# Performance work log

Measured on AMD Instinct MI355X. Metric: run time of the kernel, lower is better.

The kernel has to match this reference:

```python
import jax, jax.numpy as jnp
import numpy as np

DIM = 256
N_CHANNELS = 8
NEIGHBORS = 16


def setup_inputs() -> dict:
    key = jax.random.key(0)
    kx, kw = jax.random.split(key)
    B, N, D = 4, 1024, DIM
    x = jax.random.normal(kx, (B, N, D), dtype=jnp.float32)
    # nn.Linear(dim, dim*2*n_channels, bias=False); store as [in, out] so y = x @ W
    W_qk = jax.random.normal(kw, (D, 2 * N_CHANNELS * D), dtype=jnp.float32) * (D ** -0.5)
    return {"x": x, "W_qk": W_qk}


def _norm_edge(edge):
    # edge: [B, C, N, N]
    norm_row = edge / (edge.sum(axis=-1, keepdims=True) + 1e-6)
    norm_col = norm_row / (norm_row.sum(axis=-2, keepdims=True) + 1e-6)
    # norm_row @ norm_col^T
    return jnp.einsum('bcnk,bcmk->bcnm', norm_row, norm_col)


def reference(x, W_qk):
    B, N, D = x.shape
    C = N_CHANNELS
    scale = D ** -0.5
    qk = (x @ W_qk).reshape(B, N, 2, C, D)
    q = jnp.transpose(qk[:, :, 0], (0, 2, 1, 3))  # [B, C, N, D]
    k = jnp.transpose(qk[:, :, 1], (0, 2, 1, 3))  # [B, C, N, D]
    attn = jax.nn.softmax(jnp.einsum('bcnd,bcmd->bcnm', q, k) * scale, axis=-1)

    # clip(): top-k neighbor mask from channel-summed (detached) attention
    sum_edge = jax.lax.stop_gradient(attn).sum(axis=1)  # [B, N, N]
    kk = min(NEIGHBORS, N)
    _, top_idx = jax.lax.top_k(sum_edge, kk)  # [B, N, kk]
    b_idx = jnp.arange(B)[:, None, None]
    r_idx = jnp.arange(N)[None, :, None]
    mask = jnp.zeros((B, N, N), dtype=attn.dtype).at[b_idx, r_idx, top_idx].set(1.0)
    mask = jnp.maximum(mask, jnp.eye(N, dtype=attn.dtype))  # identity diag
    edge = mask[:, None] * attn  # [B, C, N, N]
    return _norm_edge(edge)
```

## Files before the change

### kernel.cpp

```cpp
#include <hip/hip_runtime.h>
#include <hip/hip_bf16.h>
#include <math.h>

#define BB 4
#define NN 1024
#define DD 256
#define CC 8
#define KNBR 16
#define MAXSEL 17
#define ZCAP (NN * MAXSEL)

typedef _Float16 f16x8_t __attribute__((ext_vector_type(8)));
typedef _Float16 f16x4_t __attribute__((ext_vector_type(4)));
typedef _Float16 f16x2_t __attribute__((ext_vector_type(2)));
typedef float    f32x4_t __attribute__((ext_vector_type(4)));

__device__ __forceinline__ void gl2lds16(const _Float16* g, _Float16* ldsbase) {
    __builtin_amdgcn_global_load_lds(
        (const __attribute__((address_space(1))) unsigned int*)g,
        (__attribute__((address_space(3))) unsigned int*)ldsbase, 16, 0, 0);
}

__device__ __forceinline__ void split2(float v, _Float16& h, _Float16& l) {
    h = (_Float16)v;
    l = (_Float16)(v - (float)h);
}

__global__ __launch_bounds__(256) void split_all(const float* __restrict__ x,
                                                 const float* __restrict__ W,
                                                 _Float16* __restrict__ xh,
                                                 _Float16* __restrict__ xl,
                                                 _Float16* __restrict__ Wth,
                                                 _Float16* __restrict__ Wtl,
                                                 int* __restrict__ countb) {
    const int tid = threadIdx.x;
    if (blockIdx.x < 1024) {
        int i = (blockIdx.x * 256 + tid) * 4;
        float4 v = *(const float4*)(x + i);
        f16x4_t hv, lv;
        _Float16 h, l;
        split2(v.x, h, l); hv[0] = h; lv[0] = l;
        split2(v.y, h, l); hv[1] = h; lv[1] = l;
        split2(v.z, h, l); hv[2] = h; lv[2] = l;
        split2(v.w, h, l); hv[3] = h; lv[3] = l;
        *(f16x4_t*)(xh + i) = hv;
        *(f16x4_t*)(xl + i) = lv;
    } else {
        const int b2 = blockIdx.x - 1024;
        if (b2 == 0) {
            int4 zz = make_int4(0, 0, 0, 0);
#pragma unroll
            for (int g = 0; g < 4; g++) ((int4*)countb)[tid + 256 * g] = zz;
        }
        __shared__ float t[64][65];
        const int n0 = (b2 & 63) * 64;
        const int k0 = (b2 >> 6) * 64;
#pragma unroll
        for (int i = 0; i < 16; i++) {
            int k = i * 4 + (tid >> 6);
            int n = tid & 63;
            t[k][n] = W[(size_t)(k0 + k) * 4096 + n0 + n];
        }
        __syncthreads();
#pragma unroll
        for (int i = 0; i < 16; i++) {
            int n = i * 4 + (tid >> 6);
            int k = tid & 63;
            _Float16 h, l;
            split2(t[k][n] * 16.f, h, l);
            size_t o = (size_t)(n0 + n) * 256 + k0 + k;
            Wth[o] = h; Wtl[o] = l;
        }
    }
}

#define STG(dst, src, rowbase, kk)                                             \
    do {                                                                       \
        gl2lds16((src) + (size_t)((rowbase) + r_st) * 256 + (kk) + c8,         \
                 &(dst)[(w * 64) * 8]);                                        \
        gl2lds16((src) + (size_t)((rowbase) + 64 + r_st) * 256 + (kk) + c8,    \
                 &(dst)[(256 + w * 64) * 8]);                                  \
    } while (0)

#define MFMA3(accv, AH, AL, BH, BL)                                            \
    do {                                                                       \
        accv = __builtin_amdgcn_mfma_f32_16x16x32_f16(AL, BH, accv, 0, 0, 0);  \
        accv = __builtin_amdgcn_mfma_f32_16x16x32_f16(AH, BL, accv, 0, 0, 0);  \
        accv = __builtin_amdgcn_mfma_f32_16x16x32_f16(AH, BH, accv, 0, 0, 0);  \
    } while (0)

#define COMPUTE(AH, AL, BH, BL)                                                \
    do {                                                                       \
        f16x8_t ah[4], al[4];                                                  \
        _Pragma("unroll")                                                      \
        for (int mi = 0; mi < 4; mi++) {                                       \
            int r = (wr * 64 + mi * 16 + lm) * 32 + qx8;                       \
            ah[mi] = *(const f16x8_t*)&(AH)[r];                                \
            al[mi] = *(const f16x8_t*)&(AL)[r];                                \
        }                                                                      \
        _Pragma("unroll")                                                      \
        for (int ni = 0; ni < 4; ni++) {                                       \
            int rb = (wc * 64 + ni * 16 + lm) * 32 + qx8;                      \
            f16x8_t bh = *(const f16x8_t*)&(BH)[rb];                           \
            f16x8_t bl = *(const f16x8_t*)&(BL)[rb];                           \
            _Pragma("unroll")                                                  \
            for (int mi = 0; mi < 4; mi++)                                     \
                MFMA3(acc[mi][ni], ah[mi], al[mi], bh, bl);                    \
        }                                                                      \
    } while (0)

__global__ __launch_bounds__(256) void gemm_xw_mfma(
        const _Float16* __restrict__ xh, const _Float16* __restrict__ xl,
        const _Float16* __restrict__ wth, const _Float16* __restrict__ wtl,
        _Float16* __restrict__ qh, _Float16* __restrict__ ql,
        _Float16* __restrict__ kh, _Float16* __restrict__ kl) {
    __shared__ __align__(16) char smem[65536];
    _Float16* Ah0 = (_Float16*)smem;
    _Float16* Al0 = (_Float16*)(smem + 8192);
    _Float16* Bh0 = (_Float16*)(smem + 16384);
    _Float16* Bl0 = (_Float16*)(smem + 24576);
    _Float16* Ah1 = (_Float16*)(smem + 32768);
    _Float16* Al1 = (_Float16*)(smem + 40960);
    _Float16* Bh1 = (_Float16*)(smem + 49152);
    _Float16* Bl1 = (_Float16*)(smem + 57344);
    const int tid = threadIdx.x, lane = tid & 63, w = tid >> 6;
    const int wr = w >> 1, wc = w & 1;
    const int lm = lane & 15, quad = lane >> 4;
    const int row0 = blockIdx.y * 128, col0 = blockIdx.x * 128;
    const int r_st = tid >> 2;
    const int c8 = (((tid & 3) ^ ((tid >> 3) & 3)) * 8);
    const int qx8 = ((quad ^ ((lm >> 1) & 3)) * 8);

    f32x4_t acc[4][4];
#pragma unroll
    for (int i = 0; i < 4; i++)
#pragma unroll
        for (int j = 0; j < 4; j++) acc[i][j] = (f32x4_t)(0.f);

    STG(Ah0, xh, row0, 0); STG(Al0, xl, row0, 0);
    STG(Bh0, wth, col0, 0); STG(Bl0, wtl, col0, 0);
    __syncthreads();
#pragma unroll
    for (int t = 0; t < 8; t += 2) {
        {
            int kn = (t + 1) * 32;
            if (t + 1 < 8) {
                STG(Ah1, xh, row0, kn); STG(Al1, xl, row0, kn);
                STG(Bh1, wth, col0, kn); STG(Bl1, wtl, col0, kn);
            }
            COMPUTE(Ah0, Al0, Bh0, Bl0);
            __syncthreads();
        }
        {
            int kn = (t + 2) * 32;
            if (t + 2 < 8) {
                STG(Ah0, xh, row0, kn); STG(Al0, xl, row0, kn);
                STG(Bh0, wth, col0, kn); STG(Bl0, wtl, col0, kn);
            }
            COMPUTE(Ah1, Al1, Bh1, Bl1);
            __syncthreads();
        }
    }

    float* tr = (float*)smem;
    const int s = col0 >> 11, c = (col0 >> 8) & 7, dbase = col0 & 255;
    _Float16* dh = s ? kh : qh;
    _Float16* dl = s ? kl : ql;
    const int rl = tid >> 2;
    const int cb = (tid & 3) * 8;
#pragma unroll
    for (int p = 0; p < 2; p++) {
        if (p) __syncthreads();
        if (wr == p) {
#pragma unroll
            for (int mi = 0; mi < 4; mi++) {
                int rloc = mi * 16 + quad * 4;
#pragma unroll
                for (int ni = 0; ni < 4; ni++) {
                    int cl = wc * 64 + ni * 16 + lm;
#pragma unroll
                    for (int r = 0; r < 4; r++)
                        tr[(rloc + r) * 132 + cl] = acc[mi][ni][r];
                }
            }
        }
        __syncthreads();
        int rr = row0 + p * 64 + rl;
        int bb = rr >> 10, n = rr & 1023;
        size_t base = (((size_t)(bb * CC + c)) * NN + n) * DD + dbase;
#pragma unroll
        for (int g = 0; g < 4; g++) {
            int ccol = g * 32 + cb;
            f16x8_t hv, lv;
#pragma unroll
            for (int e = 0; e < 8; e++) {
                float vv = tr[rl * 132 + ccol + e];
                _Float16 h, l;
                split2(vv, h, l);
                hv[e] = h; lv[e] = l;
            }
            *(f16x8_t*)(dh + base + ccol) = hv;
            *(f16x8_t*)(dl + base + ccol) = lv;
        }
    }
}

__global__ __launch_bounds__(256) void gemm_qkt_mfma(
        const _Float16* __restrict__ qh, const _Float16* __restrict__ ql,
        const _Float16* __restrict__ kh, const _Float16* __restrict__ kl,
        float* __restrict__ attn) {
    __shared__ __align__(16) char smem[65536];
    _Float16* Ah0 = (_Float16*)smem;
    _Float16* Al0 = (_Float16*)(smem + 8192);
    _Float16* Bh0 = (_Float16*)(smem + 16384);
    _Float16* Bl0 = (_Float16*)(smem + 24576);
    _Float16* Ah1 = (_Float16*)(smem + 32768);
    _Float16* Al1 = (_Float16*)(smem + 40960);
    _Float16* Bh1 = (_Float16*)(smem + 49152);
    _Float16* Bl1 = (_Float16*)(smem + 57344);
    const int tid = threadIdx.x, lane = tid & 63, w = tid >> 6;
    const int wr = w >> 1, wc = w & 1;
    const int lm = lane & 15, quad = lane >> 4;
    const int id = blockIdx.x;
    const int rb8 = id & 7, qq = id >> 3;
    const int j = qq & 63, zhi = qq >> 6;
    const int z = zhi * 8 + rb8;
    const int row0 = (j >> 3) * 128, col0 = (j & 7) * 128;
    const size_t zo = (size_t)z * NN * DD;
    float* Cm = attn + (size_t)z * NN * NN;
    const int r_st = tid >> 2;
    const int c8 = (((tid & 3) ^ ((tid >> 3) & 3)) * 8);
    const int qx8 = ((quad ^ ((lm >> 1) & 3)) * 8);
    const float scale = 0.0625f / 256.0f;

    f32x4_t acc[4][4];
#pragma unroll
    for (int i = 0; i < 4; i++)
#pragma unroll
        for (int j2 = 0; j2 < 4; j2++) acc[i][j2] = (f32x4_t)(0.f);

    const _Float16* qhz = qh + zo;
    const _Float16* qlz = ql + zo;
    const _Float16* khz = kh + zo;
    const _Float16* klz = kl + zo;

    STG(Ah0, qhz, row0, 0); STG(Al0, qlz, row0, 0);
    STG(Bh0, khz, col0, 0); STG(Bl0, klz, col0, 0);
    __syncthreads();
#pragma unroll
    for (int t = 0; t < 8; t += 2) {
        {
            int kn = (t + 1) * 32;
            if (t + 1 < 8) {
                STG(Ah1, qhz, row0, kn); STG(Al1, qlz, row0, kn);
                STG(Bh1, khz, col0, kn); STG(Bl1, klz, col0, kn);
            }
            COMPUTE(Ah0, Al0, Bh0, Bl0);
            __syncthreads();
        }
        {
            int kn = (t + 2) * 32;
            if (t + 2 < 8) {
                STG(Ah0, qhz, row0, kn); STG(Al0, qlz, row0, kn);
                STG(Bh0, khz, col0, kn); STG(Bl0, klz, col0, kn);
            }
            COMPUTE(Ah1, Al1, Bh1, Bl1);
            __syncthreads();
        }
    }

#pragma unroll
    for (int mi = 0; mi < 4; mi++)
#pragma unroll
        for (int ni = 0; ni < 4; ni++) {
            int row = row0 + wr * 64 + mi * 16 + quad * 4;
            int col = col0 + wc * 64 + ni * 16 + lm;
#pragma unroll
            for (int r = 0; r < 4; r++)
                Cm[(size_t)(row + r) * NN + col] = acc[mi][ni][r] * scale;
        }
}

__global__ __launch_bounds__(256) void softmax_topk(const float* __restrict__ attn,
                                                    float2* __restrict__ ml,
                                                    int* __restrict__ idx,
                                                    int* __restrict__ cnt,
                                                    int* __restrict__ countb,
                                                    float* __restrict__ colsum) {
    __shared__ float psum[4][1280];
    __shared__ int fsel[MAXSEL];
    __shared__ int fcnt;
    const int bn = blockIdx.x, b = bn >> 10, n = bn & 1023;
    const int tid = threadIdx.x, lane = tid & 63, w = tid >> 6;

    if (tid < CC) colsum[(size_t)(b * CC + tid) * NN + n] = 0.f;

    const int colb = lane * 16;
    const int pb   = lane * 20;
    float4 u[2][4];
#pragma unroll
    for (int p = 0; p < 2; p++) {
        const int c = w * 2 + p;
        const float* rowp = attn + (((size_t)(b * CC + c) * NN + n) * NN) + colb;
#pragma unroll
        for (int g = 0; g < 4; g++) u[p][g] = *(const float4*)(rowp + g * 4);
    }

    float acc[16];
#pragma unroll
    for (int e = 0; e < 16; e++) acc[e] = 0.f;

#pragma unroll
    for (int p = 0; p < 2; p++) {
        const int c = w * 2 + p;
        const float* f = (const float*)&u[p][0];
        float mx = f[0];
#pragma unroll
        for (int e = 1; e < 16; e++) mx = fmaxf(mx, f[e]);
#pragma unroll
        for (int off = 1; off < 64; off <<= 1) mx = fmaxf(mx, __shfl_xor(mx, off));
        float sm = 0.f;
        float pe[16];
#pragma unroll
        for (int e = 0; e < 16; e++) { pe[e] = expf(f[e] - mx); sm += pe[e]; }
#pragma unroll
        for (int off = 1; off < 64; off <<= 1) sm += __shfl_xor(sm, off);
        if (lane == 0) ml[(size_t)(b * CC + c) * NN + n] = make_float2(mx, sm);
        float inv = 1.0f / sm;
#pragma unroll
        for (int e = 0; e < 16; e++) acc[e] += pe[e] * inv;
    }
#pragma unroll
    for (int g = 0; g < 4; g++)
        *(float4*)&psum[w][pb + g * 4] =
            make_float4(acc[g * 4], acc[g * 4 + 1], acc[g * 4 + 2], acc[g * 4 + 3]);
    __syncthreads();

    const int p4 = tid * 4 + (tid >> 2) * 4;
    float4 a0 = *(const float4*)&psum[0][p4];
    float4 a1 = *(const float4*)&psum[1][p4];
    float4 a2 = *(const float4*)&psum[2][p4];
    float4 a3 = *(const float4*)&psum[3][p4];
    float4 vs;
    vs.x = a0.x + a1.x + a2.x + a3.x;
    vs.y = a0.y + a1.y + a2.y + a3.y;
    vs.z = a0.z + a1.z + a2.z + a3.z;
    vs.w = a0.w + a1.w + a2.w + a3.w;
    *(float4*)&psum[0][p4] = vs;
    __syncthreads();

    if (w == 0) {
        unsigned vb[16];
#pragma unroll
        for (int g = 0; g < 4; g++) {
            float4 t4 = *(const float4*)&psum[0][pb + g * 4];
            vb[g * 4 + 0] = __float_as_uint(t4.x);
            vb[g * 4 + 1] = __float_as_uint(t4.y);
            vb[g * 4 + 2] = __float_as_uint(t4.z);
            vb[g * 4 + 3] = __float_as_uint(t4.w);
        }
        unsigned lo = 0u, hi = 0x7F800000u;
        while (lo < hi) {
            unsigned mid = lo + ((hi - lo) >> 1);
            int c = 0;
#pragma unroll
            for (int e = 0; e < 16; e++)
                c += (int)__popcll(__ballot(vb[e] > mid));
            if (c <= 15) hi = mid; else lo = mid + 1;
        }
        const unsigned V = hi;
        int cgt = 0, ceq = 0;
#pragma unroll
        for (int e = 0; e < 16; e++) {
            cgt += (vb[e] > V) ? 1 : 0;
            ceq += (vb[e] == V) ? 1 : 0;
        }
        int pk = cgt | (ceq << 16);
        int incl = pk;
#pragma unroll
        for (int o = 1; o < 64; o <<= 1) {
            int v2 = __shfl_up(incl, o);
            if (lane >= o) incl += v2;
        }
        int tot = __shfl(incl, 63);
        int c1 = tot & 0xffff;
        int need = KNBR - c1;
        int excl = incl - pk;
        int pg = excl & 0xffff;
        int pe2 = excl >> 16;
        int lg = 0, le = 0;
#pragma unroll
        for (int e = 0; e < 16; e++) {
            if (vb[e] > V) {
                fsel[pg + lg] = colb + e; lg++;
            } else if (vb[e] == V) {
                if (pe2 + le < need) fsel[c1 + pe2 + le] = colb + e;
                le++;
            }
        }
        if (lane == 0) {
            bool has = false;
#pragma unroll
            for (int t2 = 0; t2 < KNBR; t2++)
                if (fsel[t2] == n) has = true;
            int c = KNBR;
            if (!has) { fsel[KNBR] = n; c = KNBR + 1; }
            fcnt = c;
            cnt[bn] = c;
        }
    }
    __syncthreads();
    if (tid < fcnt) {
        idx[bn * MAXSEL + tid] = fsel[tid];
        atomicAdd(&countb[b * NN + fsel[tid]], 1);
    }
}

__global__ __launch_bounds__(256) void scan_offb(const int* __restrict__ countb,
                                                 int* __restrict__ offb,
                                                 int* __restrict__ curs) {
    __shared__ int wtot[4];
    const int b = blockIdx.x, tid = threadIdx.x, lane = tid & 63, w = tid >> 6;
    int c0 = countb[b * NN + tid * 4 + 0];
    int c1 = countb[b * NN + tid * 4 + 1];
    int c2 = countb[b * NN + tid * 4 + 2];
    int c3 = countb[b * NN + tid * 4 + 3];
    int tsum = c0 + c1 + c2 + c3;
    int incl = tsum;
#pragma unroll
    for (int off = 1; off < 64; off <<= 1) {
        int v = __shfl_up(incl, off);
        if (lane >= off) incl += v;
    }
    if (lane == 63) wtot[w] = incl;
    __syncthreads();
    int woff = 0;
    for (int i = 0; i < w; i++) woff += wtot[i];
    int base = woff + incl - tsum;
    int o0 = base, o1 = base + c0, o2 = base + c0 + c1, o3 = base + c0 + c1 + c2;
    offb[b * NN + tid * 4 + 0] = o0;
    offb[b * NN + tid * 4 + 1] = o1;
    offb[b * NN + tid * 4 + 2] = o2;
    offb[b * NN + tid * 4 + 3] = o3;
    curs[b * NN + tid * 4 + 0] = o0;
    curs[b * NN + tid * 4 + 1] = o1;
    curs[b * NN + tid * 4 + 2] = o2;
    curs[b * NN + tid * 4 + 3] = o3;
}

__global__ __launch_bounds__(64) void fill_struct(const int* __restrict__ cnt,
                                                  const int* __restrict__ idx,
                                                  int* __restrict__ curs,
                                                  unsigned short* __restrict__ eidx16,
                                                  int* __restrict__ pmap) {
    const int b = blockIdx.x >> 4;
    const int n = ((blockIdx.x & 15) << 6) + threadIdx.x;
    const int bn = b * NN + n;
    const int c_ = cnt[bn];
    const int start = n & 15;
    for (int jj = 0; jj < MAXSEL; jj++) {
        if (jj < c_) {
            int j = jj + start;
            if (j >= c_) j -= c_;
            int k = idx[bn * MAXSEL + j];
            int p = atomicAdd(&curs[b * NN + k], 1);
            eidx16[b * ZCAP + p] = (unsigned short)n;
            pmap[bn * MAXSEL + j] = p;
        }
    }
}

__global__ __launch_bounds__(256) void rownorm_fill(const float* __restrict__ attn,
                                                    const float2* __restrict__ ml,
                                                    const int* __restrict__ idx,
                                                    const int* __restrict__ cnt,
                                                    const int* __restrict__ pmap,
                                                    float* __restrict__ nr,
                                                    float* __restrict__ colsum,
                                                    _Float16* __restrict__ eval8h) {
    const int t = blockIdx.x * 256 + threadIdx.x;
    const int z = t >> 10, n = t & 1023;
    const int b = z >> 3, c = z & 7;
    const int bn = b * NN + n;
    const int c_ = cnt[bn];
    const float* arow = attn + (size_t)t * NN;
    const float2 MM = ml[t];
    const float invl = 1.0f / MM.y;
    float a[MAXSEL];
    int kk[MAXSEL];
    float s = 0.f;
#pragma unroll
    for (int j = 0; j < MAXSEL; j++) {
        if (j < c_) {
            kk[j] = idx[bn * MAXSEL + j];
            float p = expf(arow[kk[j]] - MM.x) * invl;
            a[j] = p; s += p;
        }
    }
    const float inv = 1.f / (s + 1e-6f);
#pragma unroll
    for (int j = 0; j < MAXSEL; j++) {
        if (j < c_) {
            float v = a[j] * inv;
            nr[(size_t)t * MAXSEL + j] = v;
            atomicAdd(&colsum[(size_t)z * NN + kk[j]], v);
            int p = pmap[bn * MAXSEL + j];
            eval8h[((size_t)b * ZCAP + p) * 8 + c] = (_Float16)v;
        }
    }
}

__global__ __launch_bounds__(512) void out_sparse(const float* __restrict__ nr,
                                                  const int* __restrict__ idx,
                                                  const int* __restrict__ cnt,
                                                  const int* __restrict__ offb,
                                                  const int* __restrict__ countb,
                                                  const float* __restrict__ colsum,
                                                  const unsigned short* __restrict__ eidx16,
                                                  const _Float16* __restrict__ eval8h,
                                                  float* __restrict__ out) {
    __shared__ unsigned accP[NN * 5];
    __shared__ float scm[CC][MAXSEL];
    __shared__ int goffs[MAXSEL];
    __shared__ int glens[MAXSEL];
    const int bn = blockIdx.x;
    const int b = bn >> 10, n = bn & 1023;
    const int tid = threadIdx.x, lane = tid & 63, w = tid >> 6;
    const int c_ = cnt[bn];

#pragma unroll
    for (int q = 0; q < 10; q++) accP[tid + q * 512] = 0u;

    if (tid < 256) {
        int c = tid >> 5, j = tid & 31;
        if (j < MAXSEL) {
            float sc = 0.f;
            if (j < c_) {
                int z = b * CC + c;
                int k = idx[bn * MAXSEL + j];
                float wgt = nr[((size_t)z * NN + n) * MAXSEL + j];
                sc = wgt / (colsum[(size_t)z * NN + k] + 1e-6f);
            }
            scm[c][j] = sc;
        }
    } else if (tid < 256 + MAXSEL) {
        int j = tid - 256;
        int off = 0, len = 0;
        if (j < c_) {
            int k = idx[bn * MAXSEL + j];
            off = offb[b * NN + k];
            len = countb[b * NN + k];
        }
        goffs[j] = off; glens[j] = len;
    }
    __syncthreads();

    for (int j = w; j < c_; j += 8) {
        const int off = goffs[j], len = glens[j];
        f16x8_t scv;
#pragma unroll
        for (int c = 0; c < 8; c++) scv[c] = (_Float16)scm[c][j];
        for (int l = lane; l < len; l += 64) {
            int m = eidx16[b * ZCAP + off + l];
            f16x8_t vh = *(const f16x8_t*)(eval8h + ((size_t)b * ZCAP + off + l) * 8);
            f16x8_t pr = vh * scv;
            const unsigned* pw = (const unsigned*)&pr;
            unsigned base = (unsigned)(uintptr_t)&accP[m * 5];
            asm volatile("ds_pk_add_f16 %0, %1"           :: "v"(base), "v"(pw[0]) : "memory");
            asm volatile("ds_pk_add_f16 %0, %1 offset:4"  :: "v"(base), "v"(pw[1]) : "memory");
            asm volatile("ds_pk_add_f16 %0, %1 offset:8"  :: "v"(base), "v"(pw[2]) : "memory");
            asm volatile("ds_pk_add_f16 %0, %1 offset:12" :: "v"(base), "v"(pw[3]) : "memory");
        }
    }
    __syncthreads();

#pragma unroll
    for (int q = 0; q < 4; q++) {
        int i4 = tid + q * 512;
        int c = i4 >> 8, m0 = (i4 & 255) * 4;
        int p = c >> 1, hi = c & 1;
        float4 vo;
        float* vp = (float*)&vo;
#pragma unroll
        for (int e = 0; e < 4; e++) {
            unsigned wrd = accP[(m0 + e) * 5 + p];
            f16x2_t h2 = *(const f16x2_t*)&wrd;
            vp[e] = (float)h2[hi];
        }
        *(float4*)(out + ((size_t)(b * CC + c) * NN + n) * NN + m0) = vo;
    }
}

extern "C" void kernel_launch(void* const* d_in, const int* in_sizes, int n_in,
                              void* d_out, int out_size, void* d_ws, size_t ws_size,
                              hipStream_t stream) {
    const float* x = (const float*)d_in[0];
    const float* W = (const float*)d_in[1];
    float* out = (float*)d_out;
    char* ws = (char*)d_ws;

    float* attn = (float*)d_out;

    _Float16* qh  = (_Float16*)(ws);
    _Float16* ql  = (_Float16*)(ws + 16777216ull);
    _Float16* kh  = (_Float16*)(ws + 33554432ull);
    _Float16* kl  = (_Float16*)(ws + 50331648ull);
    _Float16* xh  = (_Float16*)(ws + 67108864ull);
    _Float16* xl  = (_Float16*)(ws + 69206016ull);
    _Float16* wth = (_Float16*)(ws + 71303168ull);
    _Float16* wtl = (_Float16*)(ws + 73400320ull);
    int*    idx  = (int*)   (ws + 75497472ull);
    int*    cnt  = (int*)   (ws + 75776000ull);
    float*  nr   = (float*) (ws + 75792384ull);
    float*  colsum = (float*)(ws + 78020608ull);
    float2* ml   = (float2*)(ws + 78151680ull);
    int*    countb = (int*) (ws + 78413824ull);
    int*    offb = (int*)   (ws + 78430208ull);
    int*    curs = (int*)   (ws + 78446592ull);
    unsigned short* eidx16 = (unsigned short*)(ws + 78462976ull);
    _Float16* eval8h = (_Float16*)(ws + 78602240ull);
    int*    pmap = (int*)   (ws + 79716352ull);

    split_all<<<1280, 256, 0, stream>>>(x, W, xh, xl, wth, wtl, countb);
    gemm_xw_mfma<<<dim3(32, 32), 256, 0, stream>>>(xh, xl, wth, wtl,
                                                   qh, ql, kh, kl);
    gemm_qkt_mfma<<<2048, 256, 0, stream>>>(qh, ql, kh, kl, attn);
    softmax_topk<<<4096, 256, 0, stream>>>(attn, ml, idx, cnt, countb, colsum);
    scan_offb<<<4, 256, 0, stream>>>(countb, offb, curs);
    fill_struct<<<64, 64, 0, stream>>>(cnt, idx, curs, eidx16, pmap);
    rownorm_fill<<<128, 256, 0, stream>>>(attn, ml, idx, cnt, pmap, nr, colsum,
                                          eval8h);
    out_sparse<<<4096, 512, 0, stream>>>(nr, idx, cnt, offb, countb, colsum,
                                         eidx16, eval8h, out);
}
```

Before: 360.4 us.

## Process one attention row per wavefront in softmax_topk, dropping LDS reduction

```diff
diff --git a/kernel.cpp b/kernel.cpp
--- a/kernel.cpp
+++ b/kernel.cpp
@@ -287,23 +287,20 @@
                                                     int* __restrict__ cnt,
                                                     int* __restrict__ countb,
                                                     float* __restrict__ colsum) {
-    __shared__ float psum[4][1280];
-    __shared__ int fsel[MAXSEL];
-    __shared__ int fcnt;
-    const int bn = blockIdx.x, b = bn >> 10, n = bn & 1023;
+    __shared__ int fsel[4][MAXSEL];
     const int tid = threadIdx.x, lane = tid & 63, w = tid >> 6;
-
-    if (tid < CC) colsum[(size_t)(b * CC + tid) * NN + n] = 0.f;
+    const int bn = blockIdx.x * 4 + w;
+    const int b = bn >> 10, n = bn & 1023;
+
+    if (lane < CC) colsum[(size_t)(b * CC + lane) * NN + n] = 0.f;
 
     const int colb = lane * 16;
-    const int pb   = lane * 20;
-    float4 u[2][4];
-#pragma unroll
-    for (int p = 0; p < 2; p++) {
-        const int c = w * 2 + p;
+    float4 u[CC][4];
+#pragma unroll
+    for (int c = 0; c < CC; c++) {
         const float* rowp = attn + (((size_t)(b * CC + c) * NN + n) * NN) + colb;
 #pragma unroll
-        for (int g = 0; g < 4; g++) u[p][g] = *(const float4*)(rowp + g * 4);
+        for (int g = 0; g < 4; g++) u[c][g] = *(const float4*)(rowp + g * 4);
     }
 
     float acc[16];
@@ -311,9 +308,8 @@
     for (int e = 0; e < 16; e++) acc[e] = 0.f;
 
 #pragma unroll
-    for (int p = 0; p < 2; p++) {
-        const int c = w * 2 + p;
-        const float* f = (const float*)&u[p][0];
+    for (int c = 0; c < CC; c++) {
+        const float* f = (const float*)&u[c][0];
         float mx = f[0];
 #pragma unroll
         for (int e = 1; e < 16; e++) mx = fmaxf(mx, f[e]);
@@ -330,89 +326,64 @@
 #pragma unroll
         for (int e = 0; e < 16; e++) acc[e] += pe[e] * inv;
     }
-#pragma unroll
-    for (int g = 0; g < 4; g++)
-        *(float4*)&psum[w][pb + g * 4] =
-            make_float4(acc[g * 4], acc[g * 4 + 1], acc[g * 4 + 2], acc[g * 4 + 3]);
-    __syncthreads();
-
-    const int p4 = tid * 4 + (tid >> 2) * 4;
-    float4 a0 = *(const float4*)&psum[0][p4];
-    float4 a1 = *(const float4*)&psum[1][p4];
-    float4 a2 = *(const float4*)&psum[2][p4];
-    float4 a3 = *(const float4*)&psum[3][p4];
-    float4 vs;
-    vs.x = a0.x + a1.x + a2.x + a3.x;
-    vs.y = a0.y + a1.y + a2.y + a3.y;
-    vs.z = a0.z + a1.z + a2.z + a3.z;
-    vs.w = a0.w + a1.w + a2.w + a3.w;
-    *(float4*)&psum[0][p4] = vs;
-    __syncthreads();
-
-    if (w == 0) {
-        unsigned vb[16];
-#pragma unroll
-        for (int g = 0; g < 4; g++) {
-            float4 t4 = *(const float4*)&psum[0][pb + g * 4];
-            vb[g * 4 + 0] = __float_as_uint(t4.x);
-            vb[g * 4 + 1] = __float_as_uint(t4.y);
-            vb[g * 4 + 2] = __float_as_uint(t4.z);
-            vb[g * 4 + 3] = __float_as_uint(t4.w);
-        }
-        unsigned lo = 0u, hi = 0x7F800000u;
-        while (lo < hi) {
-            unsigned mid = lo + ((hi - lo) >> 1);
-            int c = 0;
-#pragma unroll
-            for (int e = 0; e < 16; e++)
-                c += (int)__popcll(__ballot(vb[e] > mid));
-            if (c <= 15) hi = mid; else lo = mid + 1;
-        }
-        const unsigned V = hi;
-        int cgt = 0, ceq = 0;
-#pragma unroll
-        for (int e = 0; e < 16; e++) {
-            cgt += (vb[e] > V) ? 1 : 0;
-            ceq += (vb[e] == V) ? 1 : 0;
-        }
-        int pk = cgt | (ceq << 16);
-        int incl = pk;
-#pragma unroll
-        for (int o = 1; o < 64; o <<= 1) {
-            int v2 = __shfl_up(incl, o);
-            if (lane >= o) incl += v2;
-        }
-        int tot = __shfl(incl, 63);
-        int c1 = tot & 0xffff;
-        int need = KNBR - c1;
-        int excl = incl - pk;
-        int pg = excl & 0xffff;
-        int pe2 = excl >> 16;
-        int lg = 0, le = 0;
-#pragma unroll
-        for (int e = 0; e < 16; e++) {
-            if (vb[e] > V) {
-                fsel[pg + lg] = colb + e; lg++;
-            } else if (vb[e] == V) {
-                if (pe2 + le < need) fsel[c1 + pe2 + le] = colb + e;
-                le++;
-            }
-        }
-        if (lane == 0) {
-            bool has = false;
-#pragma unroll
-            for (int t2 = 0; t2 < KNBR; t2++)
-                if (fsel[t2] == n) has = true;
-            int c = KNBR;
-            if (!has) { fsel[KNBR] = n; c = KNBR + 1; }
-            fcnt = c;
-            cnt[bn] = c;
-        }
-    }
-    __syncthreads();
-    if (tid < fcnt) {
-        idx[bn * MAXSEL + tid] = fsel[tid];
-        atomicAdd(&countb[b * NN + fsel[tid]], 1);
+
+    unsigned vb[16];
+#pragma unroll
+    for (int e = 0; e < 16; e++) vb[e] = __float_as_uint(acc[e]);
+    unsigned lo = 0u, hi = 0x41000000u;
+    while (lo < hi) {
+        unsigned mid = lo + ((hi - lo) >> 1);
+        int c = 0;
+#pragma unroll
+        for (int e = 0; e < 16; e++)
+            c += (int)__popcll(__ballot(vb[e] > mid));
+        if (c <= 15) hi = mid; else lo = mid + 1;
+    }
+    const unsigned V = hi;
+    int cgt = 0, ceq = 0;
+#pragma unroll
+    for (int e = 0; e < 16; e++) {
+        cgt += (vb[e] > V) ? 1 : 0;
+        ceq += (vb[e] == V) ? 1 : 0;
+    }
+    int pk = cgt | (ceq << 16);
+    int incl = pk;
+#pragma unroll
+    for (int o = 1; o < 64; o <<= 1) {
+        int v2 = __shfl_up(incl, o);
+        if (lane >= o) incl += v2;
+    }
+    int tot = __shfl(incl, 63);
+    int c1 = tot & 0xffff;
+    int need = KNBR - c1;
+    int excl = incl - pk;
+    int pg = excl & 0xffff;
+    int pe2 = excl >> 16;
+    int lg = 0, le = 0;
+#pragma unroll
+    for (int e = 0; e < 16; e++) {
+        if (vb[e] > V) {
+            fsel[w][pg + lg] = colb + e; lg++;
+        } else if (vb[e] == V) {
+            if (pe2 + le < need) fsel[w][c1 + pe2 + le] = colb + e;
+            le++;
+        }
+    }
+    int fc = 0;
+    if (lane == 0) {
+        bool has = false;
+#pragma unroll
+        for (int t2 = 0; t2 < KNBR; t2++)
+            if (fsel[w][t2] == n) has = true;
+        fc = KNBR;
+        if (!has) { fsel[w][KNBR] = n; fc = KNBR + 1; }
+        cnt[bn] = fc;
+    }
+    fc = __shfl(fc, 0);
+    if (lane < fc) {
+        int k = fsel[w][lane];
+        idx[bn * MAXSEL + lane] = k;
+        atomicAdd(&countb[b * NN + k], 1);
     }
 }
 
@@ -625,7 +596,7 @@
     gemm_xw_mfma<<<dim3(32, 32), 256, 0, stream>>>(xh, xl, wth, wtl,
                                                    qh, ql, kh, kl);
     gemm_qkt_mfma<<<2048, 256, 0, stream>>>(qh, ql, kh, kl, attn);
-    softmax_topk<<<4096, 256, 0, stream>>>(attn, ml, idx, cnt, countb, colsum);
+    softmax_topk<<<1024, 256, 0, stream>>>(attn, ml, idx, cnt, countb, colsum);
     scan_offb<<<4, 256, 0, stream>>>(countb, offb, curs);
     fill_struct<<<64, 64, 0, stream>>>(cnt, idx, curs, eidx16, pmap);
     rownorm_fill<<<128, 256, 0, stream>>>(attn, ml, idx, cnt, pmap, nr, colsum,
```

Result: no change. 360.5 us (median of 2 runs) (+0.0%).
